# Kernel tuning notes

Hardware: AMD Instinct MI355X
Metric: run time of the kernel (lower is better)

## Reference

```python
import jax, jax.numpy as jnp
import numpy as np

EPS = 1e-5

def conv2d(x, w, padding):
    # x: (N, Cin, H, W), w: (Cout, Cin, kh, kw)
    return jax.lax.conv_general_dilated(
        x, w, window_strides=(1, 1),
        padding=[(padding, padding), (padding, padding)],
        dimension_numbers=('NCHW', 'OIHW', 'NCHW'))

def proj_bn_relu(x, w, gamma, beta, mean, var):
    # 1x1 conv + BatchNorm (eval mode, running stats) + ReLU
    y = conv2d(x, w, 0)
    scale = (gamma / jnp.sqrt(var + EPS))[None, :, None, None]
    shift = (beta - mean * gamma / jnp.sqrt(var + EPS))[None, :, None, None]
    return jax.nn.relu(y * scale + shift)

def setup_inputs() -> dict:
    key = jax.random.key(0)
    ks = jax.random.split(key, 16)
    B, Sx, Sy, C1, C2, Co, H, W, K = 2, 4, 4, 64, 64, 64, 128, 128, 3
    inp = {
        'u': jax.random.normal(ks[0], (B, Sx, C1, H, W), jnp.float32),
        'v': jax.random.normal(ks[1], (B, Sy, C2, H, W), jnp.float32),
        'pu_w': jax.random.normal(ks[2], (C1, C1, 1, 1), jnp.float32) * 0.05,
        'pu_gamma': jnp.ones((C1,), jnp.float32),
        'pu_beta': jnp.zeros((C1,), jnp.float32),
        'pu_mean': jax.random.normal(ks[3], (C1,), jnp.float32) * 0.1,
        'pu_var': jax.random.uniform(ks[4], (C1,), jnp.float32, 0.5, 1.5),
        'pv_w': jax.random.normal(ks[5], (C2, C2, 1, 1), jnp.float32) * 0.05,
        'pv_gamma': jnp.ones((C2,), jnp.float32),
        'pv_beta': jnp.zeros((C2,), jnp.float32),
        'pv_mean': jax.random.normal(ks[6], (C2,), jnp.float32) * 0.1,
        'pv_var': jax.random.uniform(ks[7], (C2,), jnp.float32, 0.5, 1.5),
        'conv_w': jax.random.normal(ks[8], (Co, C1 + C2, K, K), jnp.float32) * 0.02,
        'conv_b': jax.random.normal(ks[9], (Co,), jnp.float32) * 0.02,
    }
    return inp

def reference(u, v, pu_w, pu_gamma, pu_beta, pu_mean, pu_var,
              pv_w, pv_gamma, pv_beta, pv_mean, pv_var, conv_w, conv_b):
    B, Sx, C1, H, W = u.shape
    _, Sy, C2, _, _ = v.shape
    pad = 1
    # flatten set dims into batch for the 1x1 proj+BN+ReLU
    uf = proj_bn_relu(u.reshape(B * Sx, C1, H, W), pu_w, pu_gamma, pu_beta, pu_mean, pu_var)
    vf = proj_bn_relu(v.reshape(B * Sy, C2, H, W), pv_w, pv_gamma, pv_beta, pv_mean, pv_var)
    # conv over concat channels is linear -> split weight and broadcast-add,
    # exactly equal to conv(cat(repeat(u), repeat(v))) without materializing
    # the (B,Sx,Sy,C1+C2,H,W) tensor.
    w_u = conv_w[:, :C1]   # (Co, C1, K, K)
    w_v = conv_w[:, C1:]   # (Co, C2, K, K)
    ou = conv2d(uf, w_u, pad)  # (B*Sx, Co, Ho, Wo)
    ov = conv2d(vf, w_v, pad)  # (B*Sy, Co, Ho, Wo)
    Co, Ho, Wo = ou.shape[1], ou.shape[2], ou.shape[3]
    ou = ou.reshape(B, Sx, 1, Co, Ho, Wo)
    ov = ov.reshape(B, 1, Sy, Co, Ho, Wo)
    out = ou + ov + conv_b[None, None, None, :, None, None]
    return out  # (B, Sx, Sy, Co, Ho, Wo)
```

## Files before the change

### kernel.cpp

```cpp
#include <hip/hip_runtime.h>
#include <hip/hip_bf16.h>

#define C   64
#define Hh  128
#define Ww  128
#define HW  16384

typedef __attribute__((ext_vector_type(8))) short bf16x8;
typedef __attribute__((ext_vector_type(4))) float f32x4;

__device__ __forceinline__ unsigned short f2bf(float f) {
    unsigned u = __builtin_bit_cast(unsigned, f);
    unsigned r = (u + 0x7fff + ((u >> 16) & 1)) >> 16;
    return (unsigned short)r;
}

__global__ __launch_bounds__(256) void prep_kernel(
    const float* __restrict__ pu_w, const float* __restrict__ pu_g,
    const float* __restrict__ pu_b, const float* __restrict__ pu_m,
    const float* __restrict__ pu_v,
    const float* __restrict__ pv_w, const float* __restrict__ pv_g,
    const float* __restrict__ pv_b, const float* __restrict__ pv_m,
    const float* __restrict__ pv_v,
    const float* __restrict__ conv_w,
    short* __restrict__ pwu, short* __restrict__ pwv,
    short* __restrict__ wpu, short* __restrict__ wpv,
    float* __restrict__ shu, float* __restrict__ shv)
{
    const int idx = blockIdx.x * 256 + threadIdx.x;
    if (idx < 8192) {
        const int c  = idx >> 12;
        const int r  = idx & 4095;
        const int co = r >> 6, ci = r & 63;
        const float* w = c ? pv_w : pu_w;
        const float* g = c ? pv_g : pu_g;
        const float* vv = c ? pv_v : pu_v;
        const float scale = g[co] * rsqrtf(vv[co] + 1e-5f);
        (c ? pwv : pwu)[r] = (short)f2bf(w[co * 64 + ci] * scale);
    } else if (idx < 81920) {
        const int flat = idx - 8192;
        const int c  = flat / 36864;
        const int r  = flat % 36864;
        const int ch  = r / 18432;
        const int r2  = r % 18432;
        const int tap = r2 / 2048;
        const int r3  = r2 & 2047;
        const int co = r3 >> 5, ci = r3 & 31;
        const float src = conv_w[(size_t)(co * 128 + c * 64 + ch * 32 + ci) * 9 + tap];
        (c ? wpv : wpu)[((ch * 9 + tap) * 64 + co) * 32 + ci] = (short)f2bf(src);
    } else if (idx < 82048) {
        const int r  = idx - 81920;
        const int c  = r >> 6, co = r & 63;
        const float* g = c ? pv_g : pu_g;
        const float* b = c ? pv_b : pu_b;
        const float* m = c ? pv_m : pu_m;
        const float* vv = c ? pv_v : pu_v;
        const float scale = g[co] * rsqrtf(vv[co] + 1e-5f);
        (c ? shv : shu)[co] = b[co] - m[co] * scale;
    }
}

__global__ __launch_bounds__(256, 3) void proj_mfma(
    const float* __restrict__ xu, const float* __restrict__ xv,
    const short* __restrict__ pwu_, const short* __restrict__ pwv_,
    const float* __restrict__ shu_, const float* __restrict__ shv_,
    short* __restrict__ yu, short* __restrict__ yv)
{
    __shared__ short xs[256 * 72];
    __shared__ short pwl[64 * 72];
    __shared__ float ssh[64];

    const int img16 = blockIdx.y;
    const int sel   = img16 >> 3;
    const int img   = img16 & 7;
    const float* x      = sel ? xv   : xu;
    const short* pw     = sel ? pwv_ : pwu_;
    const float* shiftg = sel ? shv_ : shu_;
    short* y            = sel ? yv   : yu;

    const int pix0 = blockIdx.x * 256;
    const int tid  = threadIdx.x;

    const float* xi = x + (size_t)img * C * HW + pix0 + tid;
#pragma unroll 8
    for (int c2 = 0; c2 < 32; ++c2) {
        const float a = xi[(size_t)(2 * c2) * HW];
        const float b = xi[(size_t)(2 * c2 + 1) * HW];
        const int packed = (int)f2bf(a) | ((int)f2bf(b) << 16);
        *(int*)(&xs[tid * 72 + c2 * 2]) = packed;
    }
#pragma unroll
    for (int it = 0; it < 2; ++it) {
        const int idx = tid + it * 256;
        const int oct = idx & 7, co = idx >> 3;
        *(int4*)(&pwl[co * 72 + oct * 8]) = *(const int4*)(&pw[co * 64 + oct * 8]);
    }
    if (tid < 64) ssh[tid] = shiftg[tid];
    __syncthreads();

    const int wq = tid >> 6;
    const int lane = tid & 63;
    const int lx = lane & 15;
    const int q  = lane >> 4;

    f32x4 acc[4][4];
#pragma unroll
    for (int mt = 0; mt < 4; ++mt)
#pragma unroll
        for (int nt = 0; nt < 4; ++nt) acc[mt][nt] = (f32x4){0.f, 0.f, 0.f, 0.f};

#pragma unroll
    for (int kc = 0; kc < 2; ++kc) {
        bf16x8 a[4], b[4];
#pragma unroll
        for (int mt = 0; mt < 4; ++mt)
            a[mt] = *(const bf16x8*)&xs[((wq * 4 + mt) * 16 + lx) * 72 + kc * 32 + q * 8];
#pragma unroll
        for (int nt = 0; nt < 4; ++nt)
            b[nt] = *(const bf16x8*)&pwl[(nt * 16 + lx) * 72 + kc * 32 + q * 8];
#pragma unroll
        for (int mt = 0; mt < 4; ++mt)
#pragma unroll
            for (int nt = 0; nt < 4; ++nt)
                acc[mt][nt] = __builtin_amdgcn_mfma_f32_16x16x32_bf16(a[mt], b[nt], acc[mt][nt], 0, 0, 0);
    }

    __syncthreads();
#pragma unroll
    for (int mt = 0; mt < 4; ++mt)
#pragma unroll
        for (int nt = 0; nt < 4; ++nt)
#pragma unroll
            for (int r = 0; r < 4; ++r) {
                const int px = (wq * 4 + mt) * 16 + q * 4 + r;
                const int co = nt * 16 + lx;
                float vv = acc[mt][nt][r] + ssh[co];
                vv = fmaxf(vv, 0.f);
                xs[px * 72 + co] = (short)f2bf(vv);
            }
    __syncthreads();
    short* yo = y + ((size_t)img * HW + pix0) * C;
#pragma unroll
    for (int it = 0; it < 8; ++it) {
        const int idx = tid + it * 256;
        const int oct = idx & 7, px = idx >> 3;
        *(int4*)&yo[(size_t)px * C + oct * 8] = *(const int4*)&xs[px * 72 + oct * 8];
    }
}

template<bool FUSED>
__global__ __launch_bounds__(256, 4) void conv_fused(
    const short* __restrict__ act, const short* __restrict__ wp,
    const float* __restrict__ oug, const float* __restrict__ bias,
    float* __restrict__ outp)
{
    __shared__ short xs[204 * 68];
    __shared__ float ts[16 * 132];
    __shared__ float sbias[64];

    const int img = blockIdx.y;
    const int tx = blockIdx.x & 3, ty = blockIdx.x >> 2;
    const int h0 = ty * 4, w0 = tx * 32;
    const int tid = threadIdx.x;
    const int wq = tid >> 6;
    const int lane = tid & 63;
    const int lx = lane & 15;
    const int q  = lane >> 4;
    const int q8 = q * 8;

    if (FUSED && tid < 64) sbias[tid] = bias[tid];

    const short* ub = act + (size_t)img * HW * C;
    for (int idx = tid; idx < 1632; idx += 256) {
        const int oct = idx & 7;
        const int cell = idx >> 3;
        const int h = cell / 34, w = cell - h * 34;
        const int gh = h0 - 1 + h, gw = w0 - 1 + w;
        int4 v = {0, 0, 0, 0};
        if (gh >= 0 && gh < Hh && gw >= 0 && gw < Ww)
            v = *(const int4*)&ub[(size_t)(gh * Ww + gw) * C + oct * 8];
        *(int4*)(&xs[cell * 68 + oct * 8]) = v;
    }
    __syncthreads();

    f32x4 acc[4][2];
#pragma unroll
    for (int mt = 0; mt < 4; ++mt)
#pragma unroll
        for (int nt = 0; nt < 2; ++nt) acc[mt][nt] = (f32x4){0.f, 0.f, 0.f, 0.f};

#pragma unroll
    for (int ch = 0; ch < 2; ++ch)
#pragma unroll
        for (int t = 0; t < 9; ++t) {
            const int ky = t / 3;
            const int kx = t - ky * 3;
            bf16x8 a[4], b[2];
#pragma unroll
            for (int mt = 0; mt < 4; ++mt)
                a[mt] = *(const bf16x8*)&wp[(((ch * 9 + t) * 64) + mt * 16 + lx) * 32 + q8];
#pragma unroll
            for (int nt = 0; nt < 2; ++nt) {
                const int cell = (wq + ky) * 34 + nt * 16 + lx + kx;
                b[nt] = *(const bf16x8*)&xs[cell * 68 + ch * 32 + q8];
            }
#pragma unroll
            for (int mt = 0; mt < 4; ++mt)
#pragma unroll
                for (int nt = 0; nt < 2; ++nt)
                    acc[mt][nt] = __builtin_amdgcn_mfma_f32_16x16x32_bf16(a[mt], b[nt], acc[mt][nt], 0, 0, 0);
        }

    if (FUSED) {
#pragma unroll
        for (int mt = 0; mt < 4; ++mt)
#pragma unroll
            for (int nt = 0; nt < 2; ++nt)
#pragma unroll
                for (int r = 0; r < 4; ++r)
                    acc[mt][nt][r] += sbias[mt * 16 + q * 4 + r];
    }

    const int b  = img >> 2;
    const int sy = img & 3;

#pragma unroll
    for (int mt = 0; mt < 4; ++mt) {
        __syncthreads();
#pragma unroll
        for (int nt = 0; nt < 2; ++nt)
#pragma unroll
            for (int r = 0; r < 4; ++r)
                ts[(q * 4 + r) * 132 + wq * 32 + nt * 16 + lx] = acc[mt][nt][r];
        __syncthreads();
        if (!FUSED) {
            float* ob = outp + (size_t)img * C * HW;
#pragma unroll
            for (int k = 0; k < 2; ++k) {
                const int f = tid + k * 256;
                const int co = f >> 5, c2 = f & 31;
                const int px = c2 * 4;
                const int h2 = px >> 5, w2 = px & 31;
                *(f32x4*)&ob[(size_t)(mt * 16 + co) * HW + (h0 + h2) * Ww + w0 + w2] =
                    *(const f32x4*)&ts[co * 132 + c2 * 4];
            }
        } else {
#pragma unroll
            for (int k = 0; k < 2; ++k) {
                const int f = tid + k * 256;
                const int co = f >> 5, c2 = f & 31;
                const int px = c2 * 4;
                const int h2 = px >> 5, w2 = px & 31;
                const size_t off = (size_t)(mt * 16 + co) * HW + (h0 + h2) * Ww + w0 + w2;
                const f32x4 tv = *(const f32x4*)&ts[co * 132 + c2 * 4];
#pragma unroll
                for (int sx = 0; sx < 4; ++sx) {
                    const f32x4 o = *(const f32x4*)&oug[(size_t)(b * 4 + sx) * C * HW + off];
                    f32x4 rr = tv + o;
                    __builtin_nontemporal_store(rr,
                        (f32x4*)&outp[((size_t)((b * 4 + sx) * 4 + sy)) * C * HW + off]);
                }
            }
        }
    }
}

extern "C" void kernel_launch(void* const* d_in, const int* in_sizes, int n_in,
                              void* d_out, int out_size, void* d_ws, size_t ws_size,
                              hipStream_t stream)
{
    const float* u        = (const float*)d_in[0];
    const float* v        = (const float*)d_in[1];
    const float* pu_w     = (const float*)d_in[2];
    const float* pu_gamma = (const float*)d_in[3];
    const float* pu_beta  = (const float*)d_in[4];
    const float* pu_mean  = (const float*)d_in[5];
    const float* pu_var   = (const float*)d_in[6];
    const float* pv_w     = (const float*)d_in[7];
    const float* pv_gamma = (const float*)d_in[8];
    const float* pv_beta  = (const float*)d_in[9];
    const float* pv_mean  = (const float*)d_in[10];
    const float* pv_var   = (const float*)d_in[11];
    const float* conv_w   = (const float*)d_in[12];
    const float* conv_b   = (const float*)d_in[13];
    float* out = (float*)d_out;

    char* ws = (char*)d_ws;
    short* uf  = (short*)(ws);
    short* vf  = (short*)(ws + 16777216);
    float* ou  = (float*)(ws + 33554432);
    char*  aux = ws + 67108864;
    short* pwu = (short*)(aux);
    short* pwv = (short*)(aux + 8192);
    short* wpu = (short*)(aux + 16384);
    short* wpv = (short*)(aux + 90112);
    float* shu = (float*)(aux + 163840);
    float* shv = (float*)(aux + 164096);

    prep_kernel<<<321, 256, 0, stream>>>(pu_w, pu_gamma, pu_beta, pu_mean, pu_var,
                                         pv_w, pv_gamma, pv_beta, pv_mean, pv_var,
                                         conv_w, pwu, pwv, wpu, wpv, shu, shv);

    dim3 gp(64, 16);
    proj_mfma<<<gp, 256, 0, stream>>>(u, v, pwu, pwv, shu, shv, uf, vf);

    dim3 gc(128, 8);
    conv_fused<false><<<gc, 256, 0, stream>>>(uf, wpu, nullptr, nullptr, ou);
    conv_fused<true ><<<gc, 256, 0, stream>>>(vf, wpv, ou, conv_b, out);
}
```

Baseline: 263.6 us.

## Fold weight-prep kernel into projection kernel and vectorize input loads

Removes the separate prep kernel launch. Each projection block now folds the BN scale into its 1x1 weights and computes the shift itself, and the first two block rows also repack the 3x3 conv weights after finishing their main work. The input load is switched to float4 reads per thread covering four pixels. The trade-off is redundant per-block weight preparation in exchange for one fewer launch and wider global loads.

```diff
diff --git a/kernel.cpp b/kernel.cpp
--- a/kernel.cpp
+++ b/kernel.cpp
@@ -15,7 +15,8 @@
     return (unsigned short)r;
 }
 
-__global__ __launch_bounds__(256) void prep_kernel(
+__global__ __launch_bounds__(256, 3) void proj_mfma(
+    const float* __restrict__ xu, const float* __restrict__ xv,
     const float* __restrict__ pu_w, const float* __restrict__ pu_g,
     const float* __restrict__ pu_b, const float* __restrict__ pu_m,
     const float* __restrict__ pu_v,
@@ -23,47 +24,7 @@
     const float* __restrict__ pv_b, const float* __restrict__ pv_m,
     const float* __restrict__ pv_v,
     const float* __restrict__ conv_w,
-    short* __restrict__ pwu, short* __restrict__ pwv,
     short* __restrict__ wpu, short* __restrict__ wpv,
-    float* __restrict__ shu, float* __restrict__ shv)
-{
-    const int idx = blockIdx.x * 256 + threadIdx.x;
-    if (idx < 8192) {
-        const int c  = idx >> 12;
-        const int r  = idx & 4095;
-        const int co = r >> 6, ci = r & 63;
-        const float* w = c ? pv_w : pu_w;
-        const float* g = c ? pv_g : pu_g;
-        const float* vv = c ? pv_v : pu_v;
-        const float scale = g[co] * rsqrtf(vv[co] + 1e-5f);
-        (c ? pwv : pwu)[r] = (short)f2bf(w[co * 64 + ci] * scale);
-    } else if (idx < 81920) {
-        const int flat = idx - 8192;
-        const int c  = flat / 36864;
-        const int r  = flat % 36864;
-        const int ch  = r / 18432;
-        const int r2  = r % 18432;
-        const int tap = r2 / 2048;
-        const int r3  = r2 & 2047;
-        const int co = r3 >> 5, ci = r3 & 31;
-        const float src = conv_w[(size_t)(co * 128 + c * 64 + ch * 32 + ci) * 9 + tap];
-        (c ? wpv : wpu)[((ch * 9 + tap) * 64 + co) * 32 + ci] = (short)f2bf(src);
-    } else if (idx < 82048) {
-        const int r  = idx - 81920;
-        const int c  = r >> 6, co = r & 63;
-        const float* g = c ? pv_g : pu_g;
-        const float* b = c ? pv_b : pu_b;
-        const float* m = c ? pv_m : pu_m;
-        const float* vv = c ? pv_v : pu_v;
-        const float scale = g[co] * rsqrtf(vv[co] + 1e-5f);
-        (c ? shv : shu)[co] = b[co] - m[co] * scale;
-    }
-}
-
-__global__ __launch_bounds__(256, 3) void proj_mfma(
-    const float* __restrict__ xu, const float* __restrict__ xv,
-    const short* __restrict__ pwu_, const short* __restrict__ pwv_,
-    const float* __restrict__ shu_, const float* __restrict__ shv_,
     short* __restrict__ yu, short* __restrict__ yv)
 {
     __shared__ short xs[256 * 72];
@@ -73,29 +34,45 @@
     const int img16 = blockIdx.y;
     const int sel   = img16 >> 3;
     const int img   = img16 & 7;
-    const float* x      = sel ? xv   : xu;
-    const short* pw     = sel ? pwv_ : pwu_;
-    const float* shiftg = sel ? shv_ : shu_;
-    short* y            = sel ? yv   : yu;
+    const float* x  = sel ? xv   : xu;
+    const float* pw = sel ? pv_w : pu_w;
+    const float* pg = sel ? pv_g : pu_g;
+    const float* pb = sel ? pv_b : pu_b;
+    const float* pm = sel ? pv_m : pu_m;
+    const float* pv = sel ? pv_v : pu_v;
+    short* y        = sel ? yv   : yu;
 
     const int pix0 = blockIdx.x * 256;
     const int tid  = threadIdx.x;
 
-    const float* xi = x + (size_t)img * C * HW + pix0 + tid;
-#pragma unroll 8
-    for (int c2 = 0; c2 < 32; ++c2) {
-        const float a = xi[(size_t)(2 * c2) * HW];
-        const float b = xi[(size_t)(2 * c2 + 1) * HW];
-        const int packed = (int)f2bf(a) | ((int)f2bf(b) << 16);
-        *(int*)(&xs[tid * 72 + c2 * 2]) = packed;
-    }
-#pragma unroll
-    for (int it = 0; it < 2; ++it) {
-        const int idx = tid + it * 256;
-        const int oct = idx & 7, co = idx >> 3;
-        *(int4*)(&pwl[co * 72 + oct * 8]) = *(const int4*)(&pw[co * 64 + oct * 8]);
-    }
-    if (tid < 64) ssh[tid] = shiftg[tid];
+    for (int e = tid; e < 2048; e += 256) {
+        const int co = e >> 5;
+        const int ci0 = (e & 31) * 2;
+        const float scale = pg[co] * rsqrtf(pv[co] + 1e-5f);
+        const int packed = (int)f2bf(pw[co * 64 + ci0] * scale)
+                         | ((int)f2bf(pw[co * 64 + ci0 + 1] * scale) << 16);
+        *(int*)&pwl[co * 72 + ci0] = packed;
+    }
+    if (tid < 64) {
+        const float scale = pg[tid] * rsqrtf(pv[tid] + 1e-5f);
+        ssh[tid] = pb[tid] - pm[tid] * scale;
+    }
+
+    const float* xb = x + (size_t)img * C * HW;
+    const int qd = tid & 63;
+    const int cp = tid >> 6;
+#pragma unroll
+    for (int k = 0; k < 8; ++k) {
+        const int pairIdx = cp * 8 + k;
+        const int ci0 = pairIdx * 2;
+        const f32x4 a = *(const f32x4*)&xb[(size_t)ci0 * HW + pix0 + qd * 4];
+        const f32x4 b = *(const f32x4*)&xb[(size_t)(ci0 + 1) * HW + pix0 + qd * 4];
+#pragma unroll
+        for (int j = 0; j < 4; ++j) {
+            const int packed = (int)f2bf(a[j]) | ((int)f2bf(b[j]) << 16);
+            *(int*)&xs[(qd * 4 + j) * 72 + ci0] = packed;
+        }
+    }
     __syncthreads();
 
     const int wq = tid >> 6;
@@ -145,6 +122,20 @@
         const int idx = tid + it * 256;
         const int oct = idx & 7, px = idx >> 3;
         *(int4*)&yo[(size_t)px * C + oct * 8] = *(const int4*)&xs[px * 72 + oct * 8];
+    }
+
+    if (img16 < 2) {
+        short* wpx = img16 ? wpv : wpu;
+        const int c = img16;
+        for (int idx = blockIdx.x * 256 + tid; idx < 36864; idx += 64 * 256) {
+            const int ci = idx & 31;
+            const int co = (idx >> 5) & 63;
+            const int r3 = idx >> 11;
+            const int tap = r3 % 9;
+            const int ch  = r3 / 9;
+            const float src = conv_w[(size_t)(co * 128 + c * 64 + ch * 32 + ci) * 9 + tap];
+            wpx[idx] = (short)f2bf(src);
+        }
     }
 }
 
@@ -290,19 +281,14 @@
     short* vf  = (short*)(ws + 16777216);
     float* ou  = (float*)(ws + 33554432);
     char*  aux = ws + 67108864;
-    short* pwu = (short*)(aux);
-    short* pwv = (short*)(aux + 8192);
-    short* wpu = (short*)(aux + 16384);
-    short* wpv = (short*)(aux + 90112);
-    float* shu = (float*)(aux + 163840);
-    float* shv = (float*)(aux + 164096);
-
-    prep_kernel<<<321, 256, 0, stream>>>(pu_w, pu_gamma, pu_beta, pu_mean, pu_var,
-                                         pv_w, pv_gamma, pv_beta, pv_mean, pv_var,
-                                         conv_w, pwu, pwv, wpu, wpv, shu, shv);
+    short* wpu = (short*)(aux);
+    short* wpv = (short*)(aux + 73728);
 
     dim3 gp(64, 16);
-    proj_mfma<<<gp, 256, 0, stream>>>(u, v, pwu, pwv, shu, shv, uf, vf);
+    proj_mfma<<<gp, 256, 0, stream>>>(u, v,
+                                      pu_w, pu_gamma, pu_beta, pu_mean, pu_var,
+                                      pv_w, pv_gamma, pv_beta, pv_mean, pv_var,
+                                      conv_w, wpu, wpv, uf, vf);
 
     dim3 gc(128, 8);
     conv_fused<false><<<gc, 256, 0, stream>>>(uf, wpu, nullptr, nullptr, ou);
```

Result: no change. 267.2 us (+1.4%).
